# Kernel optimization log

Hardware: AMD Instinct MI355X
Metric: run time of the kernel (lower is better)

Reference implementation:

```python
import math
import jax, jax.numpy as jnp
import numpy as np

B, S, H, NH = 2, 2048, 1024, 4
DH = H // NH


def setup_inputs() -> dict:
    key = jax.random.key(0)
    ks = jax.random.split(key, 8)
    gate_std = 1.0 / math.sqrt(3 * H)
    return {
        "q": jax.random.normal(ks[0], (B, S, H), jnp.float32),
        "k": jax.random.normal(ks[1], (B, S, H), jnp.float32),
        "v": jax.random.normal(ks[2], (B, S, H), jnp.float32),
        "w_igate": jax.random.normal(ks[3], (NH, 3 * H), jnp.float32) * gate_std,
        "b_igate": jax.random.normal(ks[4], (NH,), jnp.float32) * 0.1,
        "w_fgate": jax.random.normal(ks[5], (NH, 3 * H), jnp.float32) * gate_std,
        "b_fgate": jnp.linspace(3.4, 6.0, NH, dtype=jnp.float32),  # bias_linspace_init_
        "ln_weight": jnp.zeros((H,), jnp.float32),  # residual weight: effective scale = 1 + w
    }


def _mlstm_parallel(qh, kh, vh, ig, fg, eps=1e-6):
    # qh,kh,vh: (B,NH,S,DH); ig,fg: (B,NH,S)
    b, nh, s, dh = qh.shape
    log_f = jax.nn.log_sigmoid(fg)                       # (B,NH,S)
    pcs = jnp.pad(jnp.cumsum(log_f, axis=-1), ((0, 0), (0, 0), (1, 0)))  # (B,NH,S+1)
    mat = pcs[..., :, None] - pcs[..., None, :]          # (B,NH,S+1,S+1)
    ltr = jnp.tril(jnp.ones((s, s), dtype=bool))
    log_fg_matrix = jnp.where(ltr, mat[..., 1:, 1:], -jnp.inf)
    log_D = log_fg_matrix + ig[..., None, :]             # (B,NH,S,S)
    max_log_D = jnp.max(log_D, axis=-1, keepdims=True)   # rowwise stabilization
    D = jnp.exp(log_D - max_log_D)
    qk = jnp.einsum('bhsd,bhtd->bhst', qh, kh) / math.sqrt(dh)
    C = qk * D
    normalizer = jnp.maximum(jnp.abs(C.sum(axis=-1, keepdims=True)), jnp.exp(-max_log_D))
    Cn = C / (normalizer + eps)
    return jnp.einsum('bhst,bhtd->bhsd', Cn, vh)         # (B,NH,S,DH)


def reference(q, k, v, w_igate, b_igate, w_fgate, b_fgate, ln_weight):
    b, s, h = q.shape
    nh = b_igate.shape[0]
    dh = h // nh
    # gate preactivations from concat([q,k,v])
    gin = jnp.concatenate([q, k, v], axis=-1)            # (B,S,3H)
    ig = jnp.einsum('bsd,hd->bhs', gin, w_igate) + b_igate[None, :, None]
    fg = jnp.einsum('bsd,hd->bhs', gin, w_fgate) + b_fgate[None, :, None]
    # split heads
    qh = q.reshape(b, s, nh, dh).transpose(0, 2, 1, 3)
    kh = k.reshape(b, s, nh, dh).transpose(0, 2, 1, 3)
    vh = v.reshape(b, s, nh, dh).transpose(0, 2, 1, 3)
    hst = _mlstm_parallel(qh, kh, vh, ig, fg)            # (B,NH,S,DH)
    # MultiHeadLayerNorm: group_norm over DH per head (biased variance), scale = 1 + ln_weight
    mean = hst.mean(axis=-1, keepdims=True)
    var = hst.var(axis=-1, keepdims=True)
    hn = (hst - mean) / jnp.sqrt(var + 1e-5)
    scale = (1.0 + ln_weight).reshape(nh, dh)
    hn = hn * scale[None, :, None, :]
    return hn.transpose(0, 2, 1, 3).reshape(b, s, h)
```

## Files before the change

kernel.cpp:

```cpp
#include <hip/hip_runtime.h>
#include <hip/hip_bf16.h>
#include <cstddef>

constexpr int Bx = 2, Sx = 2048, Hx = 1024, NHx = 4, DHx = 256;
constexpr float RSQ = 0.0625f;

typedef __attribute__((ext_vector_type(8))) short    bf16x8;
typedef __attribute__((ext_vector_type(4))) float    f32x4;
typedef __attribute__((ext_vector_type(4))) unsigned u32x4;

__device__ __forceinline__ float logsigf(float x) {
  return (x >= 0.0f) ? -log1pf(expf(-x)) : x - log1pf(expf(x));
}
__device__ __forceinline__ unsigned short f2bf(float x) {
  unsigned u = __builtin_bit_cast(unsigned, x);
  u = (u + 0x7fffu + ((u >> 16) & 1u)) >> 16;
  return (unsigned short)u;
}
__device__ __forceinline__ float bf2f(unsigned short u) {
  unsigned v = (unsigned)u << 16;
  return __builtin_bit_cast(float, v);
}
__device__ __forceinline__ unsigned pk2bf(float a, float b) {
  return (unsigned)f2bf(a) | ((unsigned)f2bf(b) << 16);
}

__device__ __forceinline__ size_t kaddr(int bh, int spos, int d) {
  return ((size_t)(bh * 64 + (spos >> 5))) * 16384
       + ((spos >> 4) & 1) * 4096 + (d >> 5) * 512 + (spos & 15) * 32
       + ((d >> 3) & 3) * 8 + (d & 7);
}

__global__ __launch_bounds__(512)
void gates_kernel(const float* __restrict__ q, const float* __restrict__ k,
                  const float* __restrict__ v,
                  const float* __restrict__ wi, const float* __restrict__ bi,
                  const float* __restrict__ wf, const float* __restrict__ bf,
                  float* __restrict__ ig, float* __restrict__ fg,
                  unsigned short* __restrict__ Qb, unsigned short* __restrict__ KVt)
{
  const int w = threadIdx.x >> 6, l = threadIdx.x & 63;
  const int bs0 = blockIdx.x * 16;
  const int bsr0 = bs0 + w * 2, bsr1 = bsr0 + 1;
  float p[2][8];
#pragma unroll
  for (int rr = 0; rr < 2; ++rr)
#pragma unroll
    for (int g2 = 0; g2 < 8; ++g2) p[rr][g2] = 0.f;

#pragma unroll
  for (int chunk = 0; chunk < 12; ++chunk) {
    const int idx = l * 4 + chunk * 256;
    const float* src; int off;
    if (idx < 1024)       { src = q; off = idx; }
    else if (idx < 2048)  { src = k; off = idx - 1024; }
    else                  { src = v; off = idx - 2048; }
    float4 g0 = *(const float4*)(src + (size_t)bsr0 * Hx + off);
    float4 g1 = *(const float4*)(src + (size_t)bsr1 * Hx + off);
#pragma unroll
    for (int h = 0; h < 4; ++h) {
      float4 wiv = *(const float4*)(wi + h * 3 * Hx + idx);
      float4 wfv = *(const float4*)(wf + h * 3 * Hx + idx);
      p[0][h]     += g0.x*wiv.x + g0.y*wiv.y + g0.z*wiv.z + g0.w*wiv.w;
      p[1][h]     += g1.x*wiv.x + g1.y*wiv.y + g1.z*wiv.z + g1.w*wiv.w;
      p[0][4 + h] += g0.x*wfv.x + g0.y*wfv.y + g0.z*wfv.z + g0.w*wfv.w;
      p[1][4 + h] += g1.x*wfv.x + g1.y*wfv.y + g1.z*wfv.z + g1.w*wfv.w;
    }
    if (idx < 2048) {
      const int hh = off >> 8, dd = off & 255;
      const int b0 = bsr0 >> 11, s0p = bsr0 & 2047;
      const int b1 = bsr1 >> 11, s1p = bsr1 & 2047;
      ushort4 o0; o0.x=f2bf(g0.x); o0.y=f2bf(g0.y); o0.z=f2bf(g0.z); o0.w=f2bf(g0.w);
      ushort4 o1; o1.x=f2bf(g1.x); o1.y=f2bf(g1.y); o1.z=f2bf(g1.z); o1.w=f2bf(g1.w);
      if (idx < 1024) {
        *(ushort4*)(Qb + ((size_t)(b0 * NHx + hh) * Sx + s0p) * DHx + dd) = o0;
        *(ushort4*)(Qb + ((size_t)(b1 * NHx + hh) * Sx + s1p) * DHx + dd) = o1;
      } else {
        *(ushort4*)(KVt + kaddr(b0 * NHx + hh, s0p, dd)) = o0;
        *(ushort4*)(KVt + kaddr(b1 * NHx + hh, s1p, dd)) = o1;
      }
    }
  }
#pragma unroll
  for (int rr = 0; rr < 2; ++rr)
#pragma unroll
    for (int g2 = 0; g2 < 8; ++g2) {
      float x = p[rr][g2];
      x += __shfl_xor(x, 1);  x += __shfl_xor(x, 2);  x += __shfl_xor(x, 4);
      x += __shfl_xor(x, 8);  x += __shfl_xor(x, 16); x += __shfl_xor(x, 32);
      p[rr][g2] = x;
    }
  if (l == 0) {
#pragma unroll
    for (int rr = 0; rr < 2; ++rr) {
      const int bs = bs0 + w * 2 + rr;
      const int b = bs >> 11, spos = bs & 2047;
#pragma unroll
      for (int h = 0; h < 4; ++h) {
        ig[(size_t)(b * NHx + h) * Sx + spos] = p[rr][h] + bi[h];
        fg[(size_t)(b * NHx + h) * Sx + spos] = p[rr][4 + h] + bf[h];
      }
    }
  }
}

__global__ __launch_bounds__(256)
void scan_kernel(const float* __restrict__ ig, const float* __restrict__ fg,
                 float* __restrict__ av, float* __restrict__ Mv,
                 float* __restrict__ nfv)
{
  const int bh = blockIdx.x;
  const int t  = threadIdx.x;
  const size_t base = (size_t)bh * Sx;
  const int s0 = t * 8;
  float4 f0 = *(const float4*)(fg + base + s0);
  float4 f1 = *(const float4*)(fg + base + s0 + 4);
  float4 g0 = *(const float4*)(ig + base + s0);
  float4 g1 = *(const float4*)(ig + base + s0 + 4);
  float xf[8] = {f0.x,f0.y,f0.z,f0.w,f1.x,f1.y,f1.z,f1.w};
  float xi[8] = {g0.x,g0.y,g0.z,g0.w,g1.x,g1.y,g1.z,g1.w};
  float ps[8];
  float run = 0.0f;
#pragma unroll
  for (int i = 0; i < 8; ++i) { run += logsigf(xf[i]); ps[i] = run; }
  __shared__ float ssum[256];
  __shared__ float smax[256];
  ssum[t] = run;
  __syncthreads();
  for (int st = 1; st < 256; st <<= 1) {
    float addv = (t >= st) ? ssum[t - st] : 0.0f;
    __syncthreads();
    ssum[t] += addv;
    __syncthreads();
  }
  const float exs = (t > 0) ? ssum[t - 1] : 0.0f;
  float a[8], pm[8];
  float rm = -INFINITY;
#pragma unroll
  for (int i = 0; i < 8; ++i) {
    a[i] = xi[i] - (exs + ps[i]);
    rm = fmaxf(rm, a[i]);
    pm[i] = rm;
  }
  smax[t] = rm;
  __syncthreads();
  for (int st = 1; st < 256; st <<= 1) {
    float mv = (t >= st) ? smax[t - st] : -INFINITY;
    __syncthreads();
    smax[t] = fmaxf(smax[t], mv);
    __syncthreads();
  }
  const float exm = (t > 0) ? smax[t - 1] : -INFINITY;
#pragma unroll
  for (int i = 0; i < 8; ++i) {
    const float M = fmaxf(exm, pm[i]);
    const float F = exs + ps[i];
    av[base + s0 + i]  = a[i];
    Mv[base + s0 + i]  = M;
    nfv[base + s0 + i] = expf(-(F + M));
  }
}

__global__ __launch_bounds__(256)
void vtrans_kernel(const float* __restrict__ v, unsigned short* __restrict__ KVt)
{
  __shared__ float t32[32][260];
  const int tile = blockIdx.x, bh = blockIdx.y, b = bh >> 2, h = bh & 3;
  const int t = threadIdx.x;
  {
    const int r = t >> 3, dc = (t & 7) * 32;
    const float* p = v + ((size_t)b * Sx + tile * 32 + r) * Hx + h * DHx + dc;
#pragma unroll
    for (int i = 0; i < 8; ++i) {
      float4 x = *(const float4*)(p + i * 4);
      t32[r][dc + i*4 + 0] = x.x; t32[r][dc + i*4 + 1] = x.y;
      t32[r][dc + i*4 + 2] = x.z; t32[r][dc + i*4 + 3] = x.w;
    }
  }
  __syncthreads();
  {
    const int ds2 = t >> 4, llv = t & 15;
    const int d = ds2 * 16 + llv;
    unsigned short* dst = KVt + ((size_t)(bh * 64 + tile)) * 16384 + 8192
                        + ds2 * 512 + llv * 32;
#pragma unroll
    for (int g = 0; g < 8; ++g) {
      ushort4 o;
      o.x = f2bf(t32[g*4+0][d]); o.y = f2bf(t32[g*4+1][d]);
      o.z = f2bf(t32[g*4+2][d]); o.w = f2bf(t32[g*4+3][d]);
      *(ushort4*)(dst + g * 4) = o;
    }
  }
}

__global__ __launch_bounds__(512, 2)
void mlstm_pass1(const unsigned short* __restrict__ Qb,
                 const unsigned short* __restrict__ KVt,
                 const float* __restrict__ av, const float* __restrict__ Mv,
                 unsigned short* __restrict__ part, float* __restrict__ rsums)
{
  __shared__ __align__(16) unsigned short KVls[2][16384];
  __shared__ float avls[1024];

  const int bh = blockIdx.x;
  const int u  = blockIdx.y;
  const int ti = 15 - (u >> 1), c = u & 1;
  const int i0 = ti * 128;
  const int ntc = 2 * ti + 2;
  const int tj0 = c * ntc, tje = tj0 + ntc;
  const int key0 = tj0 * 32;
  const int pidx = bh * 32 + u;

  const int tid = threadIdx.x;
  const int w = tid >> 6, l = tid & 63;
  const int lg = l >> 4, ll = l & 15;
  const size_t bhS = (size_t)bh * Sx;
  const int qrow = i0 + w * 16 + ll;

  for (int i = tid; i < ntc * 32; i += 512) avls[i] = av[bhS + key0 + i];

  bf16x8 qf[8];
  {
    const unsigned short* qp = Qb + (bhS + qrow) * DHx + lg * 8;
#pragma unroll
    for (int d8 = 0; d8 < 8; ++d8) qf[d8] = *(const bf16x8*)(qp + d8 * 32);
  }
  const float Mq = Mv[bhS + qrow];

  f32x4 acc[16];
#pragma unroll
  for (int jt = 0; jt < 16; ++jt) acc[jt] = f32x4{0, 0, 0, 0};
  float rsum = 0.f;

  const unsigned short* kvb = KVt + (size_t)(bh * 64) * 16384;
  uint4 r0, r1, r2, r3;

#define LOADR(tj) {                                                        \
    const unsigned short* _s = kvb + (size_t)(tj) * 16384 + tid * 8;       \
    r0 = *(const uint4*)(_s);          r1 = *(const uint4*)(_s + 4096);    \
    r2 = *(const uint4*)(_s + 8192);   r3 = *(const uint4*)(_s + 12288); }
#define WRITER(buf) {                                                      \
    char* _d = (char*)&KVls[buf][0] + tid * 16;                            \
    *(uint4*)(_d)         = r0; *(uint4*)(_d + 8192)  = r1;                \
    *(uint4*)(_d + 16384) = r2; *(uint4*)(_d + 24576) = r3; }

  LOADR(tj0);
  asm volatile("s_waitcnt vmcnt(0)" ::: "memory");
  WRITER(0);
  LOADR(tj0 + 1);
  asm volatile("s_waitcnt lgkmcnt(0)" ::: "memory");
  __builtin_amdgcn_s_barrier();

  for (int tj = tj0; tj < tje; ++tj) {
    const int cur = (tj - tj0) & 1;
    asm volatile("s_waitcnt vmcnt(0)" ::: "memory");
    if (tj + 1 < tje) WRITER(cur ^ 1);
    if (tj + 2 < tje) LOADR(tj + 2);
    __builtin_amdgcn_sched_barrier(0);

    const char* KB = (const char*)&KVls[cur][0];
    const char* VB = KB + 16384;
    const int rel = tj * 32 - key0;

    f32x4 st0 = {0,0,0,0}, st1 = {0,0,0,0};
#pragma unroll
    for (int d8 = 0; d8 < 8; ++d8) {
      const int fo = d8 * 1024 + ll * 64 + lg * 16;
      bf16x8 k0 = *(const bf16x8*)(KB + fo);
      bf16x8 k1 = *(const bf16x8*)(KB + 8192 + fo);
      st0 = __builtin_amdgcn_mfma_f32_16x16x32_bf16(k0, qf[d8], st0, 0, 0, 0);
      st1 = __builtin_amdgcn_mfma_f32_16x16x32_bf16(k1, qf[d8], st1, 0, 0, 0);
    }
    const f32x4 a4_0 = *(const f32x4*)&avls[rel + lg * 4];
    const f32x4 a4_1 = *(const f32x4*)&avls[rel + 16 + lg * 4];

    const int j0 = tj * 32;
    unsigned x0[4], x1[4];
#pragma unroll
    for (int kt = 0; kt < 2; ++kt) {
      const f32x4 s = kt ? st1 : st0;
      const f32x4 a = kt ? a4_1 : a4_0;
      const int kb = j0 + kt * 16 + 4 * lg;
      float p0 = (kb + 0 <= qrow) ? s[0] * (RSQ * __expf(a[0] - Mq)) : 0.f;
      float p1 = (kb + 1 <= qrow) ? s[1] * (RSQ * __expf(a[1] - Mq)) : 0.f;
      float p2 = (kb + 2 <= qrow) ? s[2] * (RSQ * __expf(a[2] - Mq)) : 0.f;
      float p3 = (kb + 3 <= qrow) ? s[3] * (RSQ * __expf(a[3] - Mq)) : 0.f;
      rsum += (p0 + p1) + (p2 + p3);
      unsigned lo = pk2bf(p0, p1), hi = pk2bf(p2, p3);
      unsigned plo = __shfl_xor(lo, 16), phi = __shfl_xor(hi, 16);
      bool ge = ((lg & 1) == 0);
      unsigned* x = kt ? x1 : x0;
      x[0] = ge ? lo : plo;  x[1] = ge ? hi : phi;
      x[2] = ge ? plo : lo;  x[3] = ge ? phi : hi;
    }
    unsigned pw0, pw1, pw2, pw3;
#pragma unroll
    for (int j = 0; j < 4; ++j) {
      unsigned yA = __shfl_xor(x0[j], 32);
      unsigned yB = __shfl_xor(x1[j], 32);
      unsigned r = (lg == 0) ? x0[j] : (lg == 1) ? yA : (lg == 2) ? yB : x1[j];
      if (j == 0) pw0 = r; else if (j == 1) pw1 = r; else if (j == 2) pw2 = r; else pw3 = r;
    }
    u32x4 w4 = {pw0, pw1, pw2, pw3};
    bf16x8 pb = __builtin_bit_cast(bf16x8, w4);

#pragma unroll
    for (int ds2 = 0; ds2 < 16; ++ds2) {
      bf16x8 vf = *(const bf16x8*)(VB + ds2 * 1024 + ll * 64 + lg * 16);
      acc[ds2] = __builtin_amdgcn_mfma_f32_16x16x32_bf16(vf, pb, acc[ds2], 0, 0, 0);
    }

    asm volatile("s_waitcnt lgkmcnt(0)" ::: "memory");
    __builtin_amdgcn_sched_barrier(0);
    __builtin_amdgcn_s_barrier();
  }
#undef LOADR
#undef WRITER

  float rs = rsum;
  rs += __shfl_xor(rs, 16); rs += __shfl_xor(rs, 32);
  unsigned short* pO = part + (size_t)pidx * 32768 + (w * 16 + ll) * 256 + lg * 4;
#pragma unroll
  for (int ds2 = 0; ds2 < 16; ++ds2) {
    ushort4 o;
    o.x = f2bf(acc[ds2][0]); o.y = f2bf(acc[ds2][1]);
    o.z = f2bf(acc[ds2][2]); o.w = f2bf(acc[ds2][3]);
    *(ushort4*)(pO + ds2 * 16) = o;
  }
  if (lg == 0) rsums[pidx * 128 + w * 16 + ll] = rs;
}

__global__ __launch_bounds__(512)
void mlstm_pass2(const unsigned short* __restrict__ part,
                 const float* __restrict__ rsums,
                 const float* __restrict__ nfv, const float* __restrict__ lnw,
                 float* __restrict__ out)
{
  const int bh = blockIdx.x, b = bh >> 2, h = bh & 3;
  const int ti = blockIdx.y;
  const int u0 = (15 - ti) * 2;
  const int p0 = bh * 32 + u0, p1 = p0 + 1;
  const int tid = threadIdx.x;
  const int q = tid >> 2, dc = (tid & 3) * 64;
  const int qrow = ti * 128 + q;
  const size_t bhS = (size_t)bh * Sx;

  const unsigned short* A  = part + (size_t)p0 * 32768 + q * 256 + dc;
  const unsigned short* Bp = part + (size_t)p1 * 32768 + q * 256 + dc;
  const float rs = rsums[p0 * 128 + q] + rsums[p1 * 128 + q];
  const float nf = nfv[bhS + qrow];
  const float inv = 1.f / (fmaxf(fabsf(rs), nf) + 1e-6f);

  float o[64];
  float s1 = 0.f, s2 = 0.f;
#pragma unroll
  for (int j = 0; j < 8; ++j) {
    bf16x8 va = *(const bf16x8*)(A + j * 8);
    bf16x8 vb = *(const bf16x8*)(Bp + j * 8);
#pragma unroll
    for (int r = 0; r < 8; ++r) {
      float x = (bf2f((unsigned short)va[r]) + bf2f((unsigned short)vb[r])) * inv;
      o[j * 8 + r] = x; s1 += x; s2 += x * x;
    }
  }
  s1 += __shfl_xor(s1, 1); s1 += __shfl_xor(s1, 2);
  s2 += __shfl_xor(s2, 1); s2 += __shfl_xor(s2, 2);
  const float mean = s1 * (1.f / 256.f);
  const float var  = s2 * (1.f / 256.f) - mean * mean;
  const float rstd = rsqrtf(var + 1e-5f);
  float* op = out + ((size_t)b * Sx + qrow) * Hx + h * DHx + dc;
#pragma unroll
  for (int j = 0; j < 16; ++j) {
    f32x4 lw = *(const f32x4*)(lnw + h * DHx + dc + j * 4);
    float4 ov;
    ov.x = (o[j*4+0] - mean) * rstd * (1.f + lw[0]);
    ov.y = (o[j*4+1] - mean) * rstd * (1.f + lw[1]);
    ov.z = (o[j*4+2] - mean) * rstd * (1.f + lw[2]);
    ov.w = (o[j*4+3] - mean) * rstd * (1.f + lw[3]);
    *(float4*)(op + j * 4) = ov;
  }
}

extern "C" void kernel_launch(void* const* d_in, const int* in_sizes, int n_in,
                              void* d_out, int out_size, void* d_ws, size_t ws_size,
                              hipStream_t stream) {
  const float* q   = (const float*)d_in[0];
  const float* k   = (const float*)d_in[1];
  const float* v   = (const float*)d_in[2];
  const float* wi  = (const float*)d_in[3];
  const float* bi  = (const float*)d_in[4];
  const float* wf  = (const float*)d_in[5];
  const float* bf  = (const float*)d_in[6];
  const float* lnw = (const float*)d_in[7];
  float* out = (float*)d_out;
  float* ws  = (float*)d_ws;

  const int G = Bx * NHx * Sx;
  float* ig  = ws;
  float* fg  = ws + (size_t)G;
  float* av  = ws + (size_t)2 * G;
  float* Mv  = ws + (size_t)3 * G;
  float* nfv = ws + (size_t)4 * G;
  unsigned short* Qb   = (unsigned short*)(ws + (size_t)5 * G);
  unsigned short* KVt  = Qb + (size_t)8388608;
  unsigned short* part = KVt + (size_t)8388608;
  float* rsums = (float*)(part + (size_t)8388608);

  gates_kernel<<<Bx * Sx / 16, 512, 0, stream>>>(q, k, v, wi, bi, wf, bf, ig, fg, Qb, KVt);
  scan_kernel<<<Bx * NHx, 256, 0, stream>>>(ig, fg, av, Mv, nfv);
  dim3 gT(64, Bx * NHx);
  vtrans_kernel<<<gT, 256, 0, stream>>>(v, KVt);
  dim3 g1(Bx * NHx, 32);
  mlstm_pass1<<<g1, 512, 0, stream>>>(Qb, KVt, av, Mv, part, rsums);
  dim3 g2(Bx * NHx, 16);
  mlstm_pass2<<<g2, 512, 0, stream>>>(part, rsums, nfv, lnw, out);
}
```

Before: 116.0 us.

## Process 256-query tiles per block with rebalanced split-K and fused last-chunk normalisation

Each wave in pass 1 now handles two 16-row query groups, so every K/V tile staged in LDS feeds twice as many MFMAs. The causal key range is split into a variable number of chunks per 256-row query tile so the 32 blocks per head stay roughly balanced. The single-chunk tile writes layer-normalised output directly, skipping the partial-buffer round trip. Pass 2 now sums a variable number of partials per query row. The cost is doubled accumulator and Q-fragment registers, which risks spills or lower occupancy, plus a larger partial buffer.

```diff
diff --git a/kernel.cpp b/kernel.cpp
--- a/kernel.cpp
+++ b/kernel.cpp
@@ -197,40 +197,54 @@
 void mlstm_pass1(const unsigned short* __restrict__ Qb,
                  const unsigned short* __restrict__ KVt,
                  const float* __restrict__ av, const float* __restrict__ Mv,
-                 unsigned short* __restrict__ part, float* __restrict__ rsums)
+                 const float* __restrict__ nfv, const float* __restrict__ lnw,
+                 unsigned short* __restrict__ part, float* __restrict__ rsums,
+                 float* __restrict__ out)
 {
   __shared__ __align__(16) unsigned short KVls[2][16384];
-  __shared__ float avls[1024];
-
-  const int bh = blockIdx.x;
-  const int u  = blockIdx.y;
-  const int ti = 15 - (u >> 1), c = u & 1;
-  const int i0 = ti * 128;
-  const int ntc = 2 * ti + 2;
-  const int tj0 = c * ntc, tje = tj0 + ntc;
+  __shared__ float avls[384];
+
+  const int bh = blockIdx.x, b = bh >> 2, h = bh & 3;
+  const int u = blockIdx.y;
+  int ti, c, nc;
+  if (u < 8)       { ti = 7; c = u;      nc = 8; }
+  else if (u < 14) { ti = 6; c = u - 8;  nc = 6; }
+  else if (u < 19) { ti = 5; c = u - 14; nc = 5; }
+  else if (u < 23) { ti = 4; c = u - 19; nc = 4; }
+  else if (u < 26) { ti = 3; c = u - 23; nc = 3; }
+  else if (u < 29) { ti = 2; c = u - 26; nc = 3; }
+  else if (u < 31) { ti = 1; c = u - 29; nc = 2; }
+  else             { ti = 0; c = 0;      nc = 1; }
+  const int ntiles = 8 * ti + 8;
+  const int tj0 = c * ntiles / nc, tje = (c + 1) * ntiles / nc;
+  const int i0 = ti * 256;
   const int key0 = tj0 * 32;
-  const int pidx = bh * 32 + u;
+  const int pidx = bh * 31 + u;
 
   const int tid = threadIdx.x;
   const int w = tid >> 6, l = tid & 63;
   const int lg = l >> 4, ll = l & 15;
   const size_t bhS = (size_t)bh * Sx;
-  const int qrow = i0 + w * 16 + ll;
-
-  for (int i = tid; i < ntc * 32; i += 512) avls[i] = av[bhS + key0 + i];
-
-  bf16x8 qf[8];
-  {
+
+  for (int i = tid; i < (tje - tj0) * 32; i += 512) avls[i] = av[bhS + key0 + i];
+
+  bf16x8 qf[2][8];
+  float Mq[2];
+#pragma unroll
+  for (int qg = 0; qg < 2; ++qg) {
+    const int qrow = i0 + w * 32 + qg * 16 + ll;
     const unsigned short* qp = Qb + (bhS + qrow) * DHx + lg * 8;
 #pragma unroll
-    for (int d8 = 0; d8 < 8; ++d8) qf[d8] = *(const bf16x8*)(qp + d8 * 32);
-  }
-  const float Mq = Mv[bhS + qrow];
-
-  f32x4 acc[16];
-#pragma unroll
-  for (int jt = 0; jt < 16; ++jt) acc[jt] = f32x4{0, 0, 0, 0};
-  float rsum = 0.f;
+    for (int d8 = 0; d8 < 8; ++d8) qf[qg][d8] = *(const bf16x8*)(qp + d8 * 32);
+    Mq[qg] = Mv[bhS + qrow];
+  }
+
+  f32x4 acc[2][16];
+#pragma unroll
+  for (int qg = 0; qg < 2; ++qg)
+#pragma unroll
+    for (int jt = 0; jt < 16; ++jt) acc[qg][jt] = f32x4{0, 0, 0, 0};
+  float rsum[2] = {0.f, 0.f};
 
   const unsigned short* kvb = KVt + (size_t)(bh * 64) * 16384;
   uint4 r0, r1, r2, r3;
@@ -260,54 +274,66 @@
 
     const char* KB = (const char*)&KVls[cur][0];
     const char* VB = KB + 16384;
-    const int rel = tj * 32 - key0;
-
-    f32x4 st0 = {0,0,0,0}, st1 = {0,0,0,0};
+    const int rel = (tj - tj0) * 32;
+
+    f32x4 st[2][2];
+#pragma unroll
+    for (int kt = 0; kt < 2; ++kt)
+#pragma unroll
+      for (int qg = 0; qg < 2; ++qg) st[kt][qg] = f32x4{0, 0, 0, 0};
 #pragma unroll
     for (int d8 = 0; d8 < 8; ++d8) {
       const int fo = d8 * 1024 + ll * 64 + lg * 16;
       bf16x8 k0 = *(const bf16x8*)(KB + fo);
       bf16x8 k1 = *(const bf16x8*)(KB + 8192 + fo);
-      st0 = __builtin_amdgcn_mfma_f32_16x16x32_bf16(k0, qf[d8], st0, 0, 0, 0);
-      st1 = __builtin_amdgcn_mfma_f32_16x16x32_bf16(k1, qf[d8], st1, 0, 0, 0);
+      st[0][0] = __builtin_amdgcn_mfma_f32_16x16x32_bf16(k0, qf[0][d8], st[0][0], 0, 0, 0);
+      st[0][1] = __builtin_amdgcn_mfma_f32_16x16x32_bf16(k0, qf[1][d8], st[0][1], 0, 0, 0);
+      st[1][0] = __builtin_amdgcn_mfma_f32_16x16x32_bf16(k1, qf[0][d8], st[1][0], 0, 0, 0);
+      st[1][1] = __builtin_amdgcn_mfma_f32_16x16x32_bf16(k1, qf[1][d8], st[1][1], 0, 0, 0);
     }
     const f32x4 a4_0 = *(const f32x4*)&avls[rel + lg * 4];
     const f32x4 a4_1 = *(const f32x4*)&avls[rel + 16 + lg * 4];
 
     const int j0 = tj * 32;
-    unsigned x0[4], x1[4];
-#pragma unroll
-    for (int kt = 0; kt < 2; ++kt) {
-      const f32x4 s = kt ? st1 : st0;
-      const f32x4 a = kt ? a4_1 : a4_0;
-      const int kb = j0 + kt * 16 + 4 * lg;
-      float p0 = (kb + 0 <= qrow) ? s[0] * (RSQ * __expf(a[0] - Mq)) : 0.f;
-      float p1 = (kb + 1 <= qrow) ? s[1] * (RSQ * __expf(a[1] - Mq)) : 0.f;
-      float p2 = (kb + 2 <= qrow) ? s[2] * (RSQ * __expf(a[2] - Mq)) : 0.f;
-      float p3 = (kb + 3 <= qrow) ? s[3] * (RSQ * __expf(a[3] - Mq)) : 0.f;
-      rsum += (p0 + p1) + (p2 + p3);
-      unsigned lo = pk2bf(p0, p1), hi = pk2bf(p2, p3);
-      unsigned plo = __shfl_xor(lo, 16), phi = __shfl_xor(hi, 16);
-      bool ge = ((lg & 1) == 0);
-      unsigned* x = kt ? x1 : x0;
-      x[0] = ge ? lo : plo;  x[1] = ge ? hi : phi;
-      x[2] = ge ? plo : lo;  x[3] = ge ? phi : hi;
-    }
-    unsigned pw0, pw1, pw2, pw3;
-#pragma unroll
-    for (int j = 0; j < 4; ++j) {
-      unsigned yA = __shfl_xor(x0[j], 32);
-      unsigned yB = __shfl_xor(x1[j], 32);
-      unsigned r = (lg == 0) ? x0[j] : (lg == 1) ? yA : (lg == 2) ? yB : x1[j];
-      if (j == 0) pw0 = r; else if (j == 1) pw1 = r; else if (j == 2) pw2 = r; else pw3 = r;
-    }
-    u32x4 w4 = {pw0, pw1, pw2, pw3};
-    bf16x8 pb = __builtin_bit_cast(bf16x8, w4);
+    bf16x8 pb[2];
+#pragma unroll
+    for (int qg = 0; qg < 2; ++qg) {
+      const int qrow = i0 + w * 32 + qg * 16 + ll;
+      unsigned x0[4], x1[4];
+#pragma unroll
+      for (int kt = 0; kt < 2; ++kt) {
+        const f32x4 s = st[kt][qg];
+        const f32x4 a = kt ? a4_1 : a4_0;
+        const int kb = j0 + kt * 16 + 4 * lg;
+        float p0 = (kb + 0 <= qrow) ? s[0] * (RSQ * __expf(a[0] - Mq[qg])) : 0.f;
+        float p1 = (kb + 1 <= qrow) ? s[1] * (RSQ * __expf(a[1] - Mq[qg])) : 0.f;
+        float p2 = (kb + 2 <= qrow) ? s[2] * (RSQ * __expf(a[2] - Mq[qg])) : 0.f;
+        float p3 = (kb + 3 <= qrow) ? s[3] * (RSQ * __expf(a[3] - Mq[qg])) : 0.f;
+        rsum[qg] += (p0 + p1) + (p2 + p3);
+        unsigned lo = pk2bf(p0, p1), hi = pk2bf(p2, p3);
+        unsigned plo = __shfl_xor(lo, 16), phi = __shfl_xor(hi, 16);
+        bool ge = ((lg & 1) == 0);
+        unsigned* x = kt ? x1 : x0;
+        x[0] = ge ? lo : plo;  x[1] = ge ? hi : phi;
+        x[2] = ge ? plo : lo;  x[3] = ge ? phi : hi;
+      }
+      unsigned pw0, pw1, pw2, pw3;
+#pragma unroll
+      for (int j = 0; j < 4; ++j) {
+        unsigned yA = __shfl_xor(x0[j], 32);
+        unsigned yB = __shfl_xor(x1[j], 32);
+        unsigned r = (lg == 0) ? x0[j] : (lg == 1) ? yA : (lg == 2) ? yB : x1[j];
+        if (j == 0) pw0 = r; else if (j == 1) pw1 = r; else if (j == 2) pw2 = r; else pw3 = r;
+      }
+      u32x4 w4 = {pw0, pw1, pw2, pw3};
+      pb[qg] = __builtin_bit_cast(bf16x8, w4);
+    }
 
 #pragma unroll
     for (int ds2 = 0; ds2 < 16; ++ds2) {
       bf16x8 vf = *(const bf16x8*)(VB + ds2 * 1024 + ll * 64 + lg * 16);
-      acc[ds2] = __builtin_amdgcn_mfma_f32_16x16x32_bf16(vf, pb, acc[ds2], 0, 0, 0);
+      acc[0][ds2] = __builtin_amdgcn_mfma_f32_16x16x32_bf16(vf, pb[0], acc[0][ds2], 0, 0, 0);
+      acc[1][ds2] = __builtin_amdgcn_mfma_f32_16x16x32_bf16(vf, pb[1], acc[1][ds2], 0, 0, 0);
     }
 
     asm volatile("s_waitcnt lgkmcnt(0)" ::: "memory");
@@ -317,17 +343,53 @@
 #undef LOADR
 #undef WRITER
 
-  float rs = rsum;
-  rs += __shfl_xor(rs, 16); rs += __shfl_xor(rs, 32);
-  unsigned short* pO = part + (size_t)pidx * 32768 + (w * 16 + ll) * 256 + lg * 4;
-#pragma unroll
-  for (int ds2 = 0; ds2 < 16; ++ds2) {
-    ushort4 o;
-    o.x = f2bf(acc[ds2][0]); o.y = f2bf(acc[ds2][1]);
-    o.z = f2bf(acc[ds2][2]); o.w = f2bf(acc[ds2][3]);
-    *(ushort4*)(pO + ds2 * 16) = o;
-  }
-  if (lg == 0) rsums[pidx * 128 + w * 16 + ll] = rs;
+#pragma unroll
+  for (int qg = 0; qg < 2; ++qg) {
+    const int qloc = w * 32 + qg * 16 + ll;
+    float rs = rsum[qg];
+    rs += __shfl_xor(rs, 16); rs += __shfl_xor(rs, 32);
+    if (nc == 1) {
+      float s1 = 0.f, s2 = 0.f;
+#pragma unroll
+      for (int jt = 0; jt < 16; ++jt)
+#pragma unroll
+        for (int r = 0; r < 4; ++r) {
+          const float x = acc[qg][jt][r];
+          s1 += x; s2 += x * x;
+        }
+      s1 += __shfl_xor(s1, 16); s1 += __shfl_xor(s1, 32);
+      s2 += __shfl_xor(s2, 16); s2 += __shfl_xor(s2, 32);
+      const int qrow = i0 + qloc;
+      const float nf = nfv[bhS + qrow];
+      const float inv = 1.f / (fmaxf(fabsf(rs), nf) + 1e-6f);
+      const float mean = s1 * inv * (1.f / 256.f);
+      const float ex2  = s2 * inv * inv * (1.f / 256.f);
+      const float var  = ex2 - mean * mean;
+      const float rstd = rsqrtf(var + 1e-5f);
+      float* op = out + ((size_t)b * Sx + qrow) * Hx + h * DHx;
+#pragma unroll
+      for (int jt = 0; jt < 16; ++jt) {
+        const int dbase = jt * 16 + lg * 4;
+        f32x4 lw = *(const f32x4*)(lnw + h * DHx + dbase);
+        float4 o;
+        o.x = (acc[qg][jt][0] * inv - mean) * rstd * (1.f + lw[0]);
+        o.y = (acc[qg][jt][1] * inv - mean) * rstd * (1.f + lw[1]);
+        o.z = (acc[qg][jt][2] * inv - mean) * rstd * (1.f + lw[2]);
+        o.w = (acc[qg][jt][3] * inv - mean) * rstd * (1.f + lw[3]);
+        *(float4*)(op + dbase) = o;
+      }
+    } else {
+      unsigned short* pO = part + (size_t)pidx * 65536 + qloc * 256 + lg * 4;
+#pragma unroll
+      for (int ds2 = 0; ds2 < 16; ++ds2) {
+        ushort4 o;
+        o.x = f2bf(acc[qg][ds2][0]); o.y = f2bf(acc[qg][ds2][1]);
+        o.z = f2bf(acc[qg][ds2][2]); o.w = f2bf(acc[qg][ds2][3]);
+        *(ushort4*)(pO + ds2 * 16) = o;
+      }
+      if (lg == 0) rsums[pidx * 256 + qloc] = rs;
+    }
+  }
 }
 
 __global__ __launch_bounds__(512)
@@ -337,31 +399,38 @@
                  float* __restrict__ out)
 {
   const int bh = blockIdx.x, b = bh >> 2, h = bh & 3;
-  const int ti = blockIdx.y;
-  const int u0 = (15 - ti) * 2;
-  const int p0 = bh * 32 + u0, p1 = p0 + 1;
+  const int ti = 1 + (int)blockIdx.y;
+  const int h2 = blockIdx.z;
+  const int nc_t[8] = {1, 2, 3, 3, 4, 5, 6, 8};
+  const int u0_t[8] = {31, 29, 26, 23, 19, 14, 8, 0};
+  const int nc = nc_t[ti], u0 = u0_t[ti];
+  const int p0 = bh * 31 + u0;
   const int tid = threadIdx.x;
-  const int q = tid >> 2, dc = (tid & 3) * 64;
-  const int qrow = ti * 128 + q;
+  const int ql = h2 * 128 + (tid >> 2), dc = (tid & 3) * 64;
+  const int qrow = ti * 256 + ql;
   const size_t bhS = (size_t)bh * Sx;
 
-  const unsigned short* A  = part + (size_t)p0 * 32768 + q * 256 + dc;
-  const unsigned short* Bp = part + (size_t)p1 * 32768 + q * 256 + dc;
-  const float rs = rsums[p0 * 128 + q] + rsums[p1 * 128 + q];
+  float o[64];
+#pragma unroll
+  for (int j = 0; j < 64; ++j) o[j] = 0.f;
+  float rs = 0.f;
+  for (int cc = 0; cc < nc; ++cc) {
+    const unsigned short* A = part + (size_t)(p0 + cc) * 65536 + ql * 256 + dc;
+#pragma unroll
+    for (int j = 0; j < 8; ++j) {
+      bf16x8 va = *(const bf16x8*)(A + j * 8);
+#pragma unroll
+      for (int r = 0; r < 8; ++r) o[j * 8 + r] += bf2f((unsigned short)va[r]);
+    }
+    rs += rsums[(p0 + cc) * 256 + ql];
+  }
   const float nf = nfv[bhS + qrow];
   const float inv = 1.f / (fmaxf(fabsf(rs), nf) + 1e-6f);
-
-  float o[64];
   float s1 = 0.f, s2 = 0.f;
 #pragma unroll
-  for (int j = 0; j < 8; ++j) {
-    bf16x8 va = *(const bf16x8*)(A + j * 8);
-    bf16x8 vb = *(const bf16x8*)(Bp + j * 8);
-#pragma unroll
-    for (int r = 0; r < 8; ++r) {
-      float x = (bf2f((unsigned short)va[r]) + bf2f((unsigned short)vb[r])) * inv;
-      o[j * 8 + r] = x; s1 += x; s2 += x * x;
-    }
+  for (int j = 0; j < 64; ++j) {
+    const float x = o[j] * inv;
+    o[j] = x; s1 += x; s2 += x * x;
   }
   s1 += __shfl_xor(s1, 1); s1 += __shfl_xor(s1, 2);
   s2 += __shfl_xor(s2, 1); s2 += __shfl_xor(s2, 2);
@@ -404,14 +473,14 @@
   unsigned short* Qb   = (unsigned short*)(ws + (size_t)5 * G);
   unsigned short* KVt  = Qb + (size_t)8388608;
   unsigned short* part = KVt + (size_t)8388608;
-  float* rsums = (float*)(part + (size_t)8388608);
+  float* rsums = (float*)(part + (size_t)16252928);
 
   gates_kernel<<<Bx * Sx / 16, 512, 0, stream>>>(q, k, v, wi, bi, wf, bf, ig, fg, Qb, KVt);
   scan_kernel<<<Bx * NHx, 256, 0, stream>>>(ig, fg, av, Mv, nfv);
   dim3 gT(64, Bx * NHx);
   vtrans_kernel<<<gT, 256, 0, stream>>>(v, KVt);
   dim3 g1(Bx * NHx, 32);
-  mlstm_pass1<<<g1, 512, 0, stream>>>(Qb, KVt, av, Mv, part, rsums);
-  dim3 g2(Bx * NHx, 16);
+  mlstm_pass1<<<g1, 512, 0, stream>>>(Qb, KVt, av, Mv, nfv, lnw, part, rsums, out);
+  dim3 g2(Bx * NHx, 7, 2);
   mlstm_pass2<<<g2, 512, 0, stream>>>(part, rsums, nfv, lnw, out);
 }
```

Measured after the change: 128.8 us. +11.0%, slower.
